# Kernel tuning notes

Hardware: AMD Instinct MI355X
Metric: run time of the kernel (lower is better)

Reference implementation:

```python
import jax, jax.numpy as jnp
import numpy as np
from jax import lax

NUM_CLASSES = 80
TOPK = 13
ALPHA = 1.0
BETA = 6.0
EPS = 1e-9
P = 150000
N = 256


def _make_boxes(key, n, scale):
    k1, k2 = jax.random.split(key)
    xy = jax.random.uniform(k1, (n, 2), dtype=jnp.float32) * scale
    wh = jax.random.uniform(k2, (n, 2), dtype=jnp.float32) * (0.2 * scale) + 1.0
    return jnp.concatenate([xy, xy + wh], axis=-1)  # valid x1y1x2y2


def setup_inputs() -> dict:
    key = jax.random.key(0)
    k1, k2, k3, k4 = jax.random.split(key, 4)
    cls_pred = jax.random.uniform(k1, (P, NUM_CLASSES), dtype=jnp.float32)
    bbox_pred = _make_boxes(k2, P, 640.0)
    bbox_gt = _make_boxes(k3, N, 640.0)
    # FG labels are > 0 (code indexes cls_pred[label-1])
    label_gt = jax.random.randint(k4, (N, 1), 1, NUM_CLASSES + 1, dtype=jnp.int32)
    return {"cls_pred": cls_pred, "bbox_pred": bbox_pred, "label_gt": label_gt, "bbox_gt": bbox_gt}


def _ious(bbox1, bbox2, eps=EPS):
    # bbox1: (N,4) gt, bbox2: (P,4) pred -> (N,P)
    b1 = bbox1[:, None, :]
    b2 = bbox2[None, :, :]
    x1y1 = jnp.maximum(b1[..., 0:2], b2[..., 0:2])
    x2y2 = jnp.minimum(b1[..., 2:4], b2[..., 2:4])
    inter = jnp.clip(x2y2 - x1y1, 0.0).prod(-1)
    area1 = jnp.clip(b1[..., 2:4] - b1[..., 0:2], 0.0).prod(-1)
    area2 = jnp.clip(b2[..., 2:4] - b2[..., 0:2], 0.0).prod(-1)
    return inter / (area1 + area2 - inter + eps)


def _metrics_topk(metrics, topk, eps=EPS):
    n, num_priors = metrics.shape
    topk_vals, topk_idxs = lax.top_k(metrics, topk)  # (N,k)
    keep = topk_vals.max(axis=-1, keepdims=True) > eps
    topk_idxs = jnp.where(keep, topk_idxs, 0)
    rows = jnp.arange(n)[:, None]
    counts = jnp.zeros((n, num_priors), jnp.int32).at[rows, topk_idxs].add(1)
    is_in_topk = jnp.where(counts > 1, 0, counts)
    return is_in_topk.astype(metrics.dtype)


def reference(cls_pred, bbox_pred, label_gt, bbox_gt):
    num_priors, num_classes = cls_pred.shape
    n_gt = bbox_gt.shape[0]
    ious = _ious(bbox_gt, bbox_pred)  # (N,P)
    lbl = label_gt.reshape(-1).astype(jnp.int32)  # (N,)
    bbox_cls_scores = jnp.take(cls_pred.T, lbl - 1, axis=0)  # (N,P)
    alignment_metrics = jnp.power(bbox_cls_scores, ALPHA) * jnp.power(ious, BETA)
    mask_positive = _metrics_topk(alignment_metrics, TOPK)  # (N,P) float 0/1
    mask_positive_sum = mask_positive.sum(axis=0)  # (P,)
    # conflict resolution: priors claimed by >1 gt go to the max-iou gt.
    # Applying unconditionally equals the torch data-dependent branch.
    is_max_iou = (jnp.arange(n_gt)[:, None] == ious.argmax(axis=0)[None, :]).astype(ious.dtype)
    mask_positive = jnp.where(mask_positive_sum[None, :] > 1, is_max_iou, mask_positive)
    mask_positive_sum = mask_positive.sum(axis=0)
    assigned_gt_index = mask_positive.argmax(axis=0)  # (P,)
    assigned_labels = lbl[assigned_gt_index]  # (P,)
    assigned_cls = jax.nn.one_hot(assigned_labels - 1, num_classes, dtype=jnp.int32)
    assigned_bboxes = bbox_gt[assigned_gt_index]  # (P,4)
    assigned_labels = jnp.where(mask_positive_sum > 0, assigned_labels, 0)
    return (assigned_gt_index, assigned_labels, assigned_cls, assigned_bboxes)
```

## Files before the change

kernel.cpp:

```cpp
#include <hip/hip_runtime.h>

#define TOPK 13
#define NCLS 80
#define EPSF 1e-9f
#define NSEG 32
#define GPB  8
#define CAP3 512

typedef unsigned long long u64;

__device__ __forceinline__ u64 shfl_xor64(u64 x, int m) {
    int lo = __shfl_xor((int)(unsigned)(x & 0xFFFFFFFFull), m, 64);
    int hi = __shfl_xor((int)(unsigned)(x >> 32), m, 64);
    return ((u64)(unsigned)hi << 32) | (unsigned)lo;
}

__global__ __launch_bounds__(256) void setup(const int* __restrict__ lbl,
                                             int* __restrict__ count,
                                             int* __restrict__ firstg,
                                             int* __restrict__ gorder, int P, int N) {
    int t = threadIdx.x;
    if (blockIdx.x == 0) {
        __shared__ int key[256];
        key[t] = (t < N) ? ((lbl[t] << 8) | t) : 0x7FFFFFFF;
        __syncthreads();
        for (int k = 2; k <= 256; k <<= 1) {
            for (int j = k >> 1; j >= 1; j >>= 1) {
                int ixj = t ^ j;
                if (ixj > t) {
                    int a = key[t], b = key[ixj];
                    bool up = ((t & k) == 0);
                    if (up ? (a > b) : (a < b)) { key[t] = b; key[ixj] = a; }
                }
                __syncthreads();
            }
        }
        if (t < N) gorder[t] = key[t] & 0xFF;
    } else {
        int base = (blockIdx.x - 1) * 1024 + t * 4;
        if (base + 3 < P) {
            *(int4*)&count[base]  = make_int4(0, 0, 0, 0);
            *(int4*)&firstg[base] = make_int4(0x7FFFFFFF, 0x7FFFFFFF, 0x7FFFFFFF, 0x7FFFFFFF);
        } else {
            for (int i = base; i < P; i++) { count[i] = 0; firstg[i] = 0x7FFFFFFF; }
        }
    }
}

__global__ __launch_bounds__(512, 8) void phaseA1(const float* __restrict__ cls,
                                                  const float4* __restrict__ bboxp,
                                                  const float4* __restrict__ bboxg,
                                                  const int* __restrict__ lbl,
                                                  const int* __restrict__ gorder,
                                                  u64* __restrict__ cand,
                                                  int P, int N, int seglen) {
#pragma clang fp contract(off)
    const int s = blockIdx.x, tile = blockIdx.y, t = threadIdx.x;
    const int wv = t >> 6, lane = t & 63;
    const int pstart = s * seglen;
    int pend = pstart + seglen; if (pend > P) pend = P;

    __shared__ int pbuf[GPB][CAP3];
    __shared__ int ctr[GPB];

    float4 gb[GPB];
#pragma unroll
    for (int j = 0; j < GPB; j++) {
        int gi8 = tile * GPB + j;
        int gj = (gi8 < N) ? gorder[gi8] : -1;
        gb[j] = (gj >= 0) ? bboxg[gj] : make_float4(0.f, 0.f, 0.f, 0.f);
    }
    if (t < GPB) ctr[t] = 0;
    __syncthreads();

    auto testapp = [&](float4 pb, int p, bool force) {
#pragma unroll
        for (int j = 0; j < GPB; j++) {
            float dx = fminf(gb[j].z, pb.z) - fmaxf(gb[j].x, pb.x);
            float dy = fminf(gb[j].w, pb.w) - fmaxf(gb[j].y, pb.y);
            bool want = ((dx > 0.0f) && (dy > 0.0f)) || force;
            if (want) {
                int slot = atomicAdd(&ctr[j], 1);
                if (slot < CAP3) pbuf[j][slot] = p;
            }
        }
    };

    int p = pstart + t;
    if (p < pend) { testapp(bboxp[p], p, t < 16); p += 512; }
    for (; p + 1536 < pend; p += 2048) {
        float4 pb0 = bboxp[p];
        float4 pb1 = bboxp[p + 512];
        float4 pb2 = bboxp[p + 1024];
        float4 pb3 = bboxp[p + 1536];
        testapp(pb0, p, false);
        testapp(pb1, p + 512, false);
        testapp(pb2, p + 1024, false);
        testapp(pb3, p + 1536, false);
    }
    for (; p < pend; p += 512) testapp(bboxp[p], p, false);
    __syncthreads();

    const int gi8 = tile * GPB + wv;
    const bool myValid = gi8 < N;
    const int gj = myValid ? gorder[gi8] : 0;
    const float4 gbw = bboxg[gj];
    const float gaw = fmaxf(gbw.z - gbw.x, 0.0f) * fmaxf(gbw.w - gbw.y, 0.0f);
    const int cidx = lbl[gj] - 1;
    const int rawtotal = ctr[wv];

    u64 K[16];
#pragma unroll
    for (int k = 0; k < 16; k++) K[k] = 0ull;

    auto ins = [&](u64 key) {
        if (key > K[TOPK - 1]) {
#pragma unroll
            for (int k = TOPK - 1; k >= 1; k--) {
                bool a = key > K[k - 1];
                K[k] = a ? K[k - 1] : (key > K[k] ? key : K[k]);
            }
            if (key > K[0]) K[0] = key;
        }
    };

    auto evalk = [&](float4 pb, float sc, int pp) -> u64 {
        float pa = fmaxf(pb.z - pb.x, 0.0f) * fmaxf(pb.w - pb.y, 0.0f);
        float xx1 = fmaxf(gbw.x, pb.x), yy1 = fmaxf(gbw.y, pb.y);
        float xx2 = fminf(gbw.z, pb.z), yy2 = fminf(gbw.w, pb.w);
        float inter = fmaxf(xx2 - xx1, 0.0f) * fmaxf(yy2 - yy1, 0.0f);
        float iou = inter / (((gaw + pa) - inter) + EPSF);
        float i2 = iou * iou;
        float m = sc * ((i2 * i2) * i2);
        unsigned ub = __float_as_uint(m);
        ub ^= ((unsigned)((int)ub >> 31)) | 0x80000000u;
        return ((u64)ub << 32) | (unsigned)(0x7FFFFFFF - pp);
    };

    if (rawtotal <= CAP3) {
        int e = lane;
        for (; e + 64 < rawtotal; e += 128) {
            int pp0 = pbuf[wv][e];
            int pp1 = pbuf[wv][e + 64];
            float4 pb0 = bboxp[pp0];
            float4 pb1 = bboxp[pp1];
            float sc0 = cls[(size_t)pp0 * NCLS + cidx];
            float sc1 = cls[(size_t)pp1 * NCLS + cidx];
            u64 k0 = evalk(pb0, sc0, pp0);
            u64 k1 = evalk(pb1, sc1, pp1);
            ins(k0);
            ins(k1);
        }
        for (; e < rawtotal; e += 64) {
            int pp = pbuf[wv][e];
            float4 pb = bboxp[pp];
            float sc = cls[(size_t)pp * NCLS + cidx];
            ins(evalk(pb, sc, pp));
        }
    } else if (myValid) {
        for (int pp = pstart + lane; pp < pend; pp += 64) {
            float4 pb = bboxp[pp];
            float sc = cls[(size_t)pp * NCLS + cidx];
            ins(evalk(pb, sc, pp));
        }
    }

    for (int str = 1; str < 64; str <<= 1) {
#pragma unroll
        for (int i = 0; i < 8; i++) {
            u64 pa = shfl_xor64(K[15 - i], str);
            u64 pb = shfl_xor64(K[i], str);
            u64 a = K[i], b = K[15 - i];
            K[i]      = (a > pa) ? a : pa;
            K[15 - i] = (b > pb) ? b : pb;
        }
#pragma unroll
        for (int j = 8; j >= 1; j >>= 1) {
#pragma unroll
            for (int i = 0; i < 16; i++) {
                if ((i & j) == 0) {
                    u64 a = K[i], b = K[i | j];
                    u64 mx = (a > b) ? a : b;
                    u64 mn = (a > b) ? b : a;
                    K[i] = mx; K[i | j] = mn;
                }
            }
        }
    }

    u64 outk = 0ull;
#pragma unroll
    for (int k = 0; k < TOPK; k++) outk = (lane == k) ? K[k] : outk;
    if (lane < TOPK && myValid)
        cand[((size_t)gj * NSEG + s) * TOPK + lane] = outk;
}

__global__ __launch_bounds__(512) void phaseA2(const u64* __restrict__ cand,
                                               int* __restrict__ count,
                                               int* __restrict__ firstg) {
    const int g = blockIdx.x;
    const int t = threadIdx.x;
    const int M = NSEG * TOPK;
    __shared__ u64 kv[512];
    kv[t] = (t < M) ? cand[(size_t)g * M + t] : 0ull;
    __syncthreads();
    for (int k = 2; k <= 512; k <<= 1) {
        for (int j = k >> 1; j >= 1; j >>= 1) {
            int ixj = t ^ j;
            if (ixj > t) {
                u64 a = kv[t], b = kv[ixj];
                bool dirFwd = ((t & k) == 0);
                bool doswap = dirFwd ? (a < b) : (a > b);
                if (doswap) { kv[t] = b; kv[ixj] = a; }
            }
            __syncthreads();
        }
    }
    const unsigned encEpsHi = __float_as_uint(EPSF) | 0x80000000u;
    if (t < TOPK && (unsigned)(kv[0] >> 32) > encEpsHi) {
        int pi = 0x7FFFFFFF - (int)(unsigned)(kv[t] & 0xFFFFFFFFull);
        atomicAdd(&count[pi], 1);
        atomicMin(&firstg[pi], g);
    }
}

__global__ __launch_bounds__(256) void phaseCF(const float4* __restrict__ bboxp,
                                               const float4* __restrict__ bboxg,
                                               const int* __restrict__ lbl,
                                               const int* __restrict__ count,
                                               const int* __restrict__ firstg,
                                               float* __restrict__ out0,
                                               float* __restrict__ out1,
                                               float4* __restrict__ outcls4,
                                               float4* __restrict__ outbox4, int P, int N) {
#pragma clang fp contract(off)
    __shared__ float4 gbS[256];
    __shared__ int glS[256];
    __shared__ int clsl[256];
    int t = threadIdx.x;
    if (t < N) { gbS[t] = bboxg[t]; glS[t] = lbl[t]; }
    __syncthreads();
    int p0 = blockIdx.x * 256;
    int nloc = P - p0; if (nloc > 256) nloc = 256;
    if (t < nloc) {
        int p = p0 + t;
        int cnt = count[p];
        int gi = 0, pos = 0;
        if (cnt == 1) { gi = firstg[p]; pos = 1; }
        else if (cnt > 1) {
            float4 pb = bboxp[p];
            float pa = fmaxf(pb.z - pb.x, 0.0f) * fmaxf(pb.w - pb.y, 0.0f);
            float best = -1.0f;
            for (int g = 0; g < N; g++) {
                float4 g4 = gbS[g];
                float gar = fmaxf(g4.z - g4.x, 0.0f) * fmaxf(g4.w - g4.y, 0.0f);
                float xx1 = fmaxf(g4.x, pb.x), yy1 = fmaxf(g4.y, pb.y);
                float xx2 = fminf(g4.z, pb.z), yy2 = fminf(g4.w, pb.w);
                float inter = fmaxf(xx2 - xx1, 0.0f) * fmaxf(yy2 - yy1, 0.0f);
                float iou = inter / (((gar + pa) - inter) + EPSF);
                if (iou > best) { best = iou; gi = g; }
            }
            pos = 1;
        }
        out0[p] = (float)gi;
        out1[p] = pos ? (float)glS[gi] : 0.0f;
        clsl[t] = glS[gi] - 1;
        outbox4[p] = gbS[gi];
    }
    __syncthreads();
    for (int f = t; f < nloc * 20; f += 256) {
        int pl = f / 20, q = f - pl * 20;
        int cl = clsl[pl], c0 = q * 4;
        float4 vv = make_float4(c0 == cl ? 1.0f : 0.0f, c0 + 1 == cl ? 1.0f : 0.0f,
                                c0 + 2 == cl ? 1.0f : 0.0f, c0 + 3 == cl ? 1.0f : 0.0f);
        outcls4[(size_t)p0 * 20 + f] = vv;
    }
}

__global__ __launch_bounds__(256) void phaseC1(const float4* __restrict__ bboxp,
                                               const float4* __restrict__ bboxg,
                                               const int* __restrict__ lbl,
                                               const int* __restrict__ count,
                                               const int* __restrict__ firstg,
                                               float* __restrict__ out0,
                                               float* __restrict__ out1, int P, int N) {
#pragma clang fp contract(off)
    __shared__ float4 gbS[256];
    __shared__ int glS[256];
    if (threadIdx.x < (unsigned)N) {
        gbS[threadIdx.x] = bboxg[threadIdx.x];
        glS[threadIdx.x] = lbl[threadIdx.x];
    }
    __syncthreads();
    int p = blockIdx.x * 256 + threadIdx.x;
    if (p >= P) return;
    int cnt = count[p];
    int gi = 0, pos = 0;
    if (cnt == 1) { gi = firstg[p]; pos = 1; }
    else if (cnt > 1) {
        float4 pb = bboxp[p];
        float pa = fmaxf(pb.z - pb.x, 0.0f) * fmaxf(pb.w - pb.y, 0.0f);
        float best = -1.0f;
        for (int g = 0; g < N; g++) {
            float4 g4 = gbS[g];
            float gar = fmaxf(g4.z - g4.x, 0.0f) * fmaxf(g4.w - g4.y, 0.0f);
            float xx1 = fmaxf(g4.x, pb.x), yy1 = fmaxf(g4.y, pb.y);
            float xx2 = fminf(g4.z, pb.z), yy2 = fminf(g4.w, pb.w);
            float inter = fmaxf(xx2 - xx1, 0.0f) * fmaxf(yy2 - yy1, 0.0f);
            float iou = inter / (((gar + pa) - inter) + EPSF);
            if (iou > best) { best = iou; gi = g; }
        }
        pos = 1;
    }
    out0[p] = (float)gi;
    out1[p] = pos ? (float)glS[gi] : 0.0f;
}

__global__ __launch_bounds__(256) void phaseC2(const float4* __restrict__ bboxg,
                                               const int* __restrict__ lbl,
                                               const float* __restrict__ out0,
                                               float* __restrict__ outcls,
                                               float* __restrict__ outbox, int P, int N) {
    __shared__ float gbb[256 * 4];
    __shared__ int glS[256];
    __shared__ int clsl[256];
    __shared__ int gil[256];
    int tid = threadIdx.x;
    if (tid < N) {
        float4 b = bboxg[tid];
        gbb[tid * 4 + 0] = b.x; gbb[tid * 4 + 1] = b.y;
        gbb[tid * 4 + 2] = b.z; gbb[tid * 4 + 3] = b.w;
        glS[tid] = lbl[tid];
    }
    __syncthreads();
    int p0 = blockIdx.x * 256;
    int nloc = P - p0; if (nloc > 256) nloc = 256;
    if (tid < nloc) {
        int gi = (int)out0[p0 + tid];
        gil[tid] = gi;
        clsl[tid] = glS[gi] - 1;
    }
    __syncthreads();
    for (int f = tid; f < nloc * NCLS; f += 256) {
        int pl = f / NCLS;
        int c  = f - pl * NCLS;
        outcls[(size_t)p0 * NCLS + f] = (c == clsl[pl]) ? 1.0f : 0.0f;
    }
    for (int f = tid; f < nloc * 4; f += 256) {
        int pl = f >> 2, k = f & 3;
        outbox[(size_t)p0 * 4 + f] = gbb[gil[pl] * 4 + k];
    }
}

extern "C" void kernel_launch(void* const* d_in, const int* in_sizes, int n_in,
                              void* d_out, int out_size, void* d_ws, size_t ws_size,
                              hipStream_t stream) {
    const float* cls_pred  = (const float*)d_in[0];
    const float* bbox_pred = (const float*)d_in[1];
    const int*   label_gt  = (const int*)d_in[2];
    const float* bbox_gt   = (const float*)d_in[3];
    int P = in_sizes[1] / 4;
    int N = in_sizes[3] / 4;

    float* out    = (float*)d_out;
    float* out0   = out;
    float* out1   = out + (size_t)P;
    float* outcls = out + (size_t)2 * P;
    float* outbox = out + (size_t)82 * P;

    int pb = (P + 255) / 256;
    int seglen = (P + NSEG - 1) / NSEG;
    int gtiles = (N + GPB - 1) / GPB;
    dim3 gridA1(NSEG, gtiles);
    int setupBlocks = 1 + (P + 1023) / 1024;
    size_t candBytes = (size_t)N * NSEG * TOPK * sizeof(u64);
    size_t needWs = (size_t)P * 8 + candBytes + (size_t)N * 4 + 64;

    if (ws_size >= needWs) {
        int* count  = (int*)d_ws;
        int* firstg = count + P;
        u64* cand   = (u64*)(firstg + P);
        int* gorder = (int*)((char*)cand + candBytes);

        setup<<<setupBlocks, 256, 0, stream>>>(label_gt, count, firstg, gorder, P, N);
        phaseA1<<<gridA1, 512, 0, stream>>>(cls_pred, (const float4*)bbox_pred,
                                            (const float4*)bbox_gt, label_gt, gorder,
                                            cand, P, N, seglen);
        phaseA2<<<N, 512, 0, stream>>>(cand, count, firstg);
        phaseCF<<<pb, 256, 0, stream>>>((const float4*)bbox_pred, (const float4*)bbox_gt,
                                        label_gt, count, firstg, out0, out1,
                                        (float4*)outcls, (float4*)outbox, P, N);
    } else {
        int* count  = (int*)outbox;
        int* firstg = ((int*)outbox) + P;
        u64* cand   = (u64*)outcls;
        int* gorder = (int*)((char*)cand + candBytes);

        setup<<<setupBlocks, 256, 0, stream>>>(label_gt, count, firstg, gorder, P, N);
        phaseA1<<<gridA1, 512, 0, stream>>>(cls_pred, (const float4*)bbox_pred,
                                            (const float4*)bbox_gt, label_gt, gorder,
                                            cand, P, N, seglen);
        phaseC1<<<pb, 256, 0, stream>>>((const float4*)bbox_pred, (const float4*)bbox_gt,
                                        label_gt, count, firstg, out0, out1, P, N);
        phaseC2<<<pb, 256, 0, stream>>>((const float4*)bbox_gt, label_gt, out0,
                                        outcls, outbox, P, N);
    }
}
```

Before: 204.8 us.

## Split waves into half-wave GT slots in phaseA1 and use wave-level merge in phaseA2

In phaseA1, only half the waves do the top-k stage: each wave now serves two ground-truth boxes, with one 32-lane half per box. The half-wave butterfly merge stops before crossing halves, and 16 candidates per segment are written instead of 13. phaseA2 replaces its 512-thread shared-memory bitonic sort, with many barriers, by a single 64-lane wave doing register insertion plus a shuffle merge. This cuts sync overhead, but half of phaseA1's waves now sit idle during candidate evaluation. The fallback path also gains the phaseA2 launch that was previously missing.

```diff
diff --git a/kernel.cpp b/kernel.cpp
--- a/kernel.cpp
+++ b/kernel.cpp
@@ -6,6 +6,7 @@
 #define NSEG 32
 #define GPB  8
 #define CAP3 512
+#define SEGK 16
 
 typedef unsigned long long u64;
 
@@ -101,13 +102,18 @@
     for (; p < pend; p += 512) testapp(bboxp[p], p, false);
     __syncthreads();
 
-    const int gi8 = tile * GPB + wv;
+    if (wv >= GPB / 2) return;
+
+    const int half = lane >> 5;
+    const int l    = lane & 31;
+    const int slot = (wv << 1) | half;
+    const int gi8 = tile * GPB + slot;
     const bool myValid = gi8 < N;
     const int gj = myValid ? gorder[gi8] : 0;
     const float4 gbw = bboxg[gj];
     const float gaw = fmaxf(gbw.z - gbw.x, 0.0f) * fmaxf(gbw.w - gbw.y, 0.0f);
     const int cidx = lbl[gj] - 1;
-    const int rawtotal = ctr[wv];
+    const int rawtotal = ctr[slot];
 
     u64 K[16];
 #pragma unroll
@@ -138,10 +144,10 @@
     };
 
     if (rawtotal <= CAP3) {
-        int e = lane;
-        for (; e + 64 < rawtotal; e += 128) {
-            int pp0 = pbuf[wv][e];
-            int pp1 = pbuf[wv][e + 64];
+        int e = l;
+        for (; e + 32 < rawtotal; e += 64) {
+            int pp0 = pbuf[slot][e];
+            int pp1 = pbuf[slot][e + 32];
             float4 pb0 = bboxp[pp0];
             float4 pb1 = bboxp[pp1];
             float sc0 = cls[(size_t)pp0 * NCLS + cidx];
@@ -151,21 +157,21 @@
             ins(k0);
             ins(k1);
         }
-        for (; e < rawtotal; e += 64) {
-            int pp = pbuf[wv][e];
+        for (; e < rawtotal; e += 32) {
+            int pp = pbuf[slot][e];
             float4 pb = bboxp[pp];
             float sc = cls[(size_t)pp * NCLS + cidx];
             ins(evalk(pb, sc, pp));
         }
     } else if (myValid) {
-        for (int pp = pstart + lane; pp < pend; pp += 64) {
+        for (int pp = pstart + l; pp < pend; pp += 32) {
             float4 pb = bboxp[pp];
             float sc = cls[(size_t)pp * NCLS + cidx];
             ins(evalk(pb, sc, pp));
         }
     }
 
-    for (int str = 1; str < 64; str <<= 1) {
+    for (int str = 1; str <= 16; str <<= 1) {
 #pragma unroll
         for (int i = 0; i < 8; i++) {
             u64 pa = shfl_xor64(K[15 - i], str);
@@ -174,15 +180,15 @@
             K[i]      = (a > pa) ? a : pa;
             K[15 - i] = (b > pb) ? b : pb;
         }
+        if (str == 16) break;
 #pragma unroll
         for (int j = 8; j >= 1; j >>= 1) {
 #pragma unroll
             for (int i = 0; i < 16; i++) {
                 if ((i & j) == 0) {
                     u64 a = K[i], b = K[i | j];
-                    u64 mx = (a > b) ? a : b;
-                    u64 mn = (a > b) ? b : a;
-                    K[i] = mx; K[i | j] = mn;
+                    K[i] = (a > b) ? a : b;
+                    K[i | j] = (a > b) ? b : a;
                 }
             }
         }
@@ -190,35 +196,63 @@
 
     u64 outk = 0ull;
 #pragma unroll
-    for (int k = 0; k < TOPK; k++) outk = (lane == k) ? K[k] : outk;
-    if (lane < TOPK && myValid)
-        cand[((size_t)gj * NSEG + s) * TOPK + lane] = outk;
-}
-
-__global__ __launch_bounds__(512) void phaseA2(const u64* __restrict__ cand,
-                                               int* __restrict__ count,
-                                               int* __restrict__ firstg) {
+    for (int k = 0; k < SEGK; k++) outk = (l == k) ? K[k] : outk;
+    if (l < SEGK && myValid)
+        cand[((size_t)gj * NSEG + s) * SEGK + l] = outk;
+}
+
+__global__ __launch_bounds__(64) void phaseA2(const u64* __restrict__ cand,
+                                              int* __restrict__ count,
+                                              int* __restrict__ firstg) {
     const int g = blockIdx.x;
-    const int t = threadIdx.x;
-    const int M = NSEG * TOPK;
-    __shared__ u64 kv[512];
-    kv[t] = (t < M) ? cand[(size_t)g * M + t] : 0ull;
-    __syncthreads();
-    for (int k = 2; k <= 512; k <<= 1) {
-        for (int j = k >> 1; j >= 1; j >>= 1) {
-            int ixj = t ^ j;
-            if (ixj > t) {
-                u64 a = kv[t], b = kv[ixj];
-                bool dirFwd = ((t & k) == 0);
-                bool doswap = dirFwd ? (a < b) : (a > b);
-                if (doswap) { kv[t] = b; kv[ixj] = a; }
-            }
-            __syncthreads();
-        }
-    }
+    const int lane = threadIdx.x;
+    const u64* src = cand + (size_t)g * (NSEG * SEGK);
+
+    u64 K[16];
+#pragma unroll
+    for (int k = 0; k < 16; k++) K[k] = 0ull;
+
+#pragma unroll
+    for (int k = 0; k < (NSEG * SEGK) / 64; k++) {
+        u64 key = src[lane + (k << 6)];
+        if (key > K[TOPK - 1]) {
+#pragma unroll
+            for (int q = TOPK - 1; q >= 1; q--) {
+                bool a = key > K[q - 1];
+                K[q] = a ? K[q - 1] : (key > K[q] ? key : K[q]);
+            }
+            if (key > K[0]) K[0] = key;
+        }
+    }
+
+    for (int str = 1; str < 64; str <<= 1) {
+#pragma unroll
+        for (int i = 0; i < 8; i++) {
+            u64 pa = shfl_xor64(K[15 - i], str);
+            u64 pb = shfl_xor64(K[i], str);
+            u64 a = K[i], b = K[15 - i];
+            K[i]      = (a > pa) ? a : pa;
+            K[15 - i] = (b > pb) ? b : pb;
+        }
+#pragma unroll
+        for (int j = 8; j >= 1; j >>= 1) {
+#pragma unroll
+            for (int i = 0; i < 16; i++) {
+                if ((i & j) == 0) {
+                    u64 a = K[i], b = K[i | j];
+                    K[i] = (a > b) ? a : b;
+                    K[i | j] = (a > b) ? b : a;
+                }
+            }
+        }
+    }
+
     const unsigned encEpsHi = __float_as_uint(EPSF) | 0x80000000u;
-    if (t < TOPK && (unsigned)(kv[0] >> 32) > encEpsHi) {
-        int pi = 0x7FFFFFFF - (int)(unsigned)(kv[t] & 0xFFFFFFFFull);
+    if (lane < TOPK && (unsigned)(K[0] >> 32) > encEpsHi) {
+        u64 outk = 0ull;
+#pragma unroll
+        for (int k = 0; k < TOPK; k++) outk = (lane == k) ? K[k] : outk;
+        int pi = 0x7FFFFFFF - (int)(unsigned)(outk & 0xFFFFFFFFull);
         atomicAdd(&count[pi], 1);
         atomicMin(&firstg[pi], g);
     }
@@ -373,7 +407,7 @@
     int gtiles = (N + GPB - 1) / GPB;
     dim3 gridA1(NSEG, gtiles);
     int setupBlocks = 1 + (P + 1023) / 1024;
-    size_t candBytes = (size_t)N * NSEG * TOPK * sizeof(u64);
+    size_t candBytes = (size_t)N * NSEG * SEGK * sizeof(u64);
     size_t needWs = (size_t)P * 8 + candBytes + (size_t)N * 4 + 64;
 
     if (ws_size >= needWs) {
@@ -386,7 +420,7 @@
         phaseA1<<<gridA1, 512, 0, stream>>>(cls_pred, (const float4*)bbox_pred,
                                             (const float4*)bbox_gt, label_gt, gorder,
                                             cand, P, N, seglen);
-        phaseA2<<<N, 512, 0, stream>>>(cand, count, firstg);
+        phaseA2<<<N, 64, 0, stream>>>(cand, count, firstg);
         phaseCF<<<pb, 256, 0, stream>>>((const float4*)bbox_pred, (const float4*)bbox_gt,
                                         label_gt, count, firstg, out0, out1,
                                         (float4*)outcls, (float4*)outbox, P, N);
@@ -400,6 +434,7 @@
         phaseA1<<<gridA1, 512, 0, stream>>>(cls_pred, (const float4*)bbox_pred,
                                             (const float4*)bbox_gt, label_gt, gorder,
                                             cand, P, N, seglen);
+        phaseA2<<<N, 64, 0, stream>>>(cand, count, firstg);
         phaseC1<<<pb, 256, 0, stream>>>((const float4*)bbox_pred, (const float4*)bbox_gt,
                                         label_gt, count, firstg, out0, out1, P, N);
         phaseC2<<<pb, 256, 0, stream>>>((const float4*)bbox_gt, label_gt, out0,
```

Result: slower. 209.3 us (+2.2%).
